# Kernel optimization log

Measured on AMD Instinct MI355X. Metric: run time of the kernel, lower is better.

Reference implementation:

```python
import jax, jax.numpy as jnp
import numpy as np

B, D, CTX, H = 262144, 16, 128, 192
IN_DIM = D + CTX + 1  # 145


def _linear_init(k, fan_in, fan_out):
    bound = 1.0 / np.sqrt(fan_in)
    kw, kb = jax.random.split(k)
    W = jax.random.uniform(kw, (fan_in, fan_out), jnp.float32, -bound, bound)
    b = jax.random.uniform(kb, (fan_out,), jnp.float32, -bound, bound)
    return W, b


def setup_inputs() -> dict:
    key = jax.random.key(0)
    ks = jax.random.split(key, 7)
    W1, b1 = _linear_init(ks[0], IN_DIM, H)
    W2, b2 = _linear_init(ks[1], H, H)
    W3, b3 = _linear_init(ks[2], H, D)
    return {
        "t": jax.random.uniform(ks[3], (), jnp.float32),
        "y": jax.random.normal(ks[4], (B, D), jnp.float32),
        "logp": jnp.zeros((B,), jnp.float32),
        "h": jax.random.normal(ks[5], (B, CTX), jnp.float32),
        "eps": jax.random.normal(ks[6], (B, D), jnp.float32),
        "W1": W1, "b1": b1, "W2": W2, "b2": b2, "W3": W3, "b3": b3,
    }


def _mlp(x, W1, b1, W2, b2, W3, b3):
    # 3-layer MLP, exact (erf) GELU as torch.nn.GELU default
    x = jax.nn.gelu(x @ W1 + b1, approximate=False)
    x = jax.nn.gelu(x @ W2 + b2, approximate=False)
    return x @ W3 + b3


def reference(t, y, logp, h, eps, W1, b1, W2, b2, W3, b3):
    Bsz = y.shape[0]
    t_feat = jnp.ones((Bsz, 1), y.dtype) * t

    def f_of_y(yy):
        inp = jnp.concatenate([yy, h, t_feat], axis=1)  # (B, D+CTX+1)
        return _mlp(inp, W1, b1, W2, b2, W3, b3)  # (B, D)

    # Hutchinson: torch computes g = J^T eps then (g*eps).sum(1) = eps^T J^T eps,
    # which per-row equals eps^T J eps = dot(eps, J eps). Forward-mode JVP computes
    # f and J eps in one fused pass (same math, no explicit backward graph).
    f, Jeps = jax.jvp(f_of_y, (y,), (eps,))
    trace = jnp.sum(Jeps * eps, axis=1)  # (B,)
    dlogp = -trace
    dh = jnp.zeros_like(h)
    return (f, dlogp, dh)
```

## Files before the change

kernel.cpp:

```cpp
#include <hip/hip_runtime.h>
#include <hip/hip_bf16.h>
#include <math.h>

#define B_TOTAL 262144
#define D 16
#define CTX 128
#define H 192
#define KX 192
#define M 32
#define BLOCK 256

typedef __attribute__((ext_vector_type(8))) short bf16x8;
typedef __attribute__((ext_vector_type(4))) float f32x4;

#define MFMA(a, b, c) __builtin_amdgcn_mfma_f32_16x16x32_bf16((a), (b), (c), 0, 0, 0)

__device__ __forceinline__ unsigned short f2bf_rne(float f) {
    unsigned u = __builtin_bit_cast(unsigned, f);
    u += 0x7FFFu + ((u >> 16) & 1u);
    return (unsigned short)(u >> 16);
}
__device__ __forceinline__ void split2(float v, unsigned short& hi, unsigned short& lo) {
    unsigned u = __builtin_bit_cast(unsigned, v);
    hi = (unsigned short)(u >> 16);
    float hf = __builtin_bit_cast(float, u & 0xFFFF0000u);
    lo = f2bf_rne(v - hf);
}
__device__ __forceinline__ void gelu_pair(float x, float& a, float& gp) {
    float e    = __expf(-0.5f * x * x);
    float az   = fabsf(x) * 0.70710678118654752f;
    float t    = __builtin_amdgcn_rcpf(fmaf(0.47047f, az, 1.0f));
    float p    = t * fmaf(t, fmaf(t, 0.7478556f, -0.0958798f), 0.3480242f);
    float erfv = __builtin_copysignf(fmaf(-p, e, 1.0f), x);
    float phi  = fmaf(0.5f, erfv, 0.5f);
    gp = fmaf(0.39894228040143268f * x, e, phi);
    a  = x * phi;
}

__global__ void prep_weights(const float* __restrict__ W1,
                             const float* __restrict__ W2,
                             const float* __restrict__ W3,
                             unsigned short* __restrict__ wt)
{
    int i = blockIdx.x * 256 + threadIdx.x;
    if (i < H * KX) {
        int n = i / KX, kp = i % KX;
        float v = 0.0f;
        if (kp < 16)                       v = W1[kp * H + n];
        else if (kp == 16)                 v = W1[144 * H + n];
        else if (kp >= 32 && kp < 160)     v = W1[(kp - 16) * H + n];
        else if (kp >= 160 && kp < 176)    v = W1[(kp - 160) * H + n];
        else if (kp == 176)                v = W1[144 * H + n];
        wt[i] = f2bf_rne(v);
        return;
    }
    i -= H * KX;
    if (i < H * H) {
        int n = i / H, k = i % H;
        wt[36864 + i] = f2bf_rne(W2[k * H + n]);
        return;
    }
    i -= H * H;
    if (i < D * H) {
        int n = i / H, k = i % H;
        wt[73728 + i] = f2bf_rne(W3[k * D + n]);
    }
}

__global__ __launch_bounds__(BLOCK, 5) void odefunc_mfma(
    const float* __restrict__ t_ptr,
    const float* __restrict__ y,
    const float* __restrict__ h,
    const float* __restrict__ eps,
    const float* __restrict__ b1,
    const float* __restrict__ b2,
    const float* __restrict__ b3,
    const unsigned short* __restrict__ wt,
    float* __restrict__ out_f,
    float* __restrict__ out_dlogp,
    float* __restrict__ out_dh)
{
    __shared__ __align__(16) unsigned char smem[30208];
    unsigned short (*Xh)[200] = (unsigned short (*)[200])smem;
    unsigned short (*Tc)[72]  = (unsigned short (*)[72])(smem + 12800);
    unsigned short (*A)[200]  = (unsigned short (*)[200])smem;
    unsigned short (*U)[200]  = (unsigned short (*)[200])(smem + 17408);

    const int tid  = threadIdx.x;
    const int lane = tid & 63;
    const int wv   = tid >> 6;
    const int quad = lane >> 4;
    const int l16  = lane & 15;
    const size_t r0 = (size_t)blockIdx.x * M;

    const unsigned short* Wt1 = wt;
    const unsigned short* Wt2 = wt + 36864;
    const unsigned short* Wt3 = wt + 73728;

    {
        float4 z4 = {0.f, 0.f, 0.f, 0.f};
        #pragma unroll
        for (int i = 0; i < 4; ++i) {
            int idx = tid + i * BLOCK;
            int r = idx >> 5, c4 = (idx & 31) * 4;
            *(float4*)(out_dh + (r0 + r) * CTX + c4) = z4;
        }
    }

    {
        int task = tid >> 7, idx = tid & 127;
        int r = idx >> 2, d4 = (idx & 3) * 4;
        const float* src = task ? eps : y;
        float4 v = *(const float4*)(src + (r0 + r) * D + d4);
        ushort4 hi, lo;
        split2(v.x, hi.x, lo.x); split2(v.y, hi.y, lo.y);
        split2(v.z, hi.z, lo.z); split2(v.w, hi.w, lo.w);
        if (task == 0) { *(ushort4*)&Xh[r][d4] = hi; *(ushort4*)&Xh[r][160 + d4] = lo; }
        else           { *(ushort4*)&Tc[r][d4] = hi; *(ushort4*)&Tc[r][32 + d4] = lo; }
    }
    if (tid < M) {
        int r = tid;
        float tv = t_ptr[0];
        unsigned short thi, tlo;
        split2(tv, thi, tlo);
        ushort4 z4 = {0, 0, 0, 0};
        ushort4 t4 = {thi, 0, 0, 0};
        ushort4 l4 = {tlo, 0, 0, 0};
        *(ushort4*)&Xh[r][16]  = t4; *(ushort4*)&Xh[r][20]  = z4;
        *(ushort4*)&Xh[r][24]  = z4; *(ushort4*)&Xh[r][28]  = z4;
        *(ushort4*)&Xh[r][176] = l4; *(ushort4*)&Xh[r][180] = z4;
        *(ushort4*)&Xh[r][184] = z4; *(ushort4*)&Xh[r][188] = z4;
        *(ushort4*)&Tc[r][16]  = z4; *(ushort4*)&Tc[r][20]  = z4;
        *(ushort4*)&Tc[r][24]  = z4; *(ushort4*)&Tc[r][28]  = z4;
        *(ushort4*)&Tc[r][48]  = z4; *(ushort4*)&Tc[r][52]  = z4;
        *(ushort4*)&Tc[r][56]  = z4; *(ushort4*)&Tc[r][60]  = z4;
    }
    #pragma unroll
    for (int i = 0; i < 4; ++i) {
        int idx = tid + i * BLOCK;
        int r = idx >> 5, c4 = (idx & 31) * 4;
        float4 v = *(const float4*)(h + (r0 + r) * CTX + c4);
        ushort4 hv = { f2bf_rne(v.x), f2bf_rne(v.y), f2bf_rne(v.z), f2bf_rne(v.w) };
        *(ushort4*)&Xh[r][32 + c4] = hv;
    }
    __syncthreads();

    const f32x4 zf = {0.f, 0.f, 0.f, 0.f};

    f32x4 z[2][3], u[2][3];
    #pragma unroll
    for (int rt = 0; rt < 2; ++rt)
        #pragma unroll
        for (int j = 0; j < 3; ++j) { z[rt][j] = zf; u[rt][j] = zf; }

    bf16x8 w1f[3][6];
    #pragma unroll
    for (int j = 0; j < 3; ++j) {
        int n = (wv * 3 + j) * 16 + l16;
        #pragma unroll
        for (int kc = 0; kc < 6; ++kc)
            w1f[j][kc] = *(const bf16x8*)(Wt1 + n * KX + kc * 32 + quad * 8);
    }
    #pragma unroll
    for (int kc = 0; kc < 6; ++kc)
        #pragma unroll
        for (int rt = 0; rt < 2; ++rt) {
            bf16x8 ah = *(const bf16x8*)&Xh[rt * 16 + l16][kc * 32 + quad * 8];
            #pragma unroll
            for (int j = 0; j < 3; ++j) z[rt][j] = MFMA(ah, w1f[j][kc], z[rt][j]);
        }
    #pragma unroll
    for (int rt = 0; rt < 2; ++rt) {
        int m = rt * 16 + l16;
        bf16x8 th = *(const bf16x8*)&Tc[m][quad * 8];
        bf16x8 tl = *(const bf16x8*)&Tc[m][32 + quad * 8];
        #pragma unroll
        for (int j = 0; j < 3; ++j) {
            u[rt][j] = MFMA(th, w1f[j][0], u[rt][j]);
            u[rt][j] = MFMA(tl, w1f[j][5], u[rt][j]);
        }
    }
    __syncthreads();

    #pragma unroll
    for (int j = 0; j < 3; ++j) {
        int n = (wv * 3 + j) * 16 + l16;
        float bb = b1[n];
        #pragma unroll
        for (int rt = 0; rt < 2; ++rt)
            #pragma unroll
            for (int rg = 0; rg < 4; ++rg) {
                int m = rt * 16 + quad * 4 + rg;
                float x = z[rt][j][rg] + bb;
                float a, gp; gelu_pair(x, a, gp);
                A[m][n] = f2bf_rne(a);
                U[m][n] = f2bf_rne(u[rt][j][rg] * gp);
            }
    }
    __syncthreads();

    f32x4 z2[2][3], u2[2][3];
    #pragma unroll
    for (int rt = 0; rt < 2; ++rt)
        #pragma unroll
        for (int j = 0; j < 3; ++j) { z2[rt][j] = zf; u2[rt][j] = zf; }

    bf16x8 w2f[3][6];
    #pragma unroll
    for (int j = 0; j < 3; ++j) {
        int n = (wv * 3 + j) * 16 + l16;
        #pragma unroll
        for (int kc = 0; kc < 6; ++kc)
            w2f[j][kc] = *(const bf16x8*)(Wt2 + n * H + kc * 32 + quad * 8);
    }
    #pragma unroll
    for (int kc = 0; kc < 6; ++kc)
        #pragma unroll
        for (int rt = 0; rt < 2; ++rt) {
            int m = rt * 16 + l16, o = kc * 32 + quad * 8;
            bf16x8 av = *(const bf16x8*)&A[m][o];
            bf16x8 uv = *(const bf16x8*)&U[m][o];
            #pragma unroll
            for (int j = 0; j < 3; ++j) {
                z2[rt][j] = MFMA(av, w2f[j][kc], z2[rt][j]);
                u2[rt][j] = MFMA(uv, w2f[j][kc], u2[rt][j]);
            }
        }
    __syncthreads();

    #pragma unroll
    for (int j = 0; j < 3; ++j) {
        int n = (wv * 3 + j) * 16 + l16;
        float bb = b2[n];
        #pragma unroll
        for (int rt = 0; rt < 2; ++rt)
            #pragma unroll
            for (int rg = 0; rg < 4; ++rg) {
                int m = rt * 16 + quad * 4 + rg;
                float x = z2[rt][j][rg] + bb;
                float a, gp; gelu_pair(x, a, gp);
                A[m][n] = f2bf_rne(a);
                U[m][n] = f2bf_rne(u2[rt][j][rg] * gp);
            }
    }
    __syncthreads();

    {
        const int strm = wv & 1, rt = wv >> 1;
        const unsigned short (*P)[200] = strm ? U : A;

        bf16x8 w3f[6];
        #pragma unroll
        for (int kc = 0; kc < 6; ++kc)
            w3f[kc] = *(const bf16x8*)(Wt3 + l16 * H + kc * 32 + quad * 8);

        f32x4 acc = zf;
        #pragma unroll
        for (int kc = 0; kc < 6; ++kc) {
            bf16x8 xv = *(const bf16x8*)&P[rt * 16 + l16][kc * 32 + quad * 8];
            acc = MFMA(xv, w3f[kc], acc);
        }

        if (strm == 0) {
            float bb = b3[l16];
            #pragma unroll
            for (int rg = 0; rg < 4; ++rg) {
                int m = rt * 16 + quad * 4 + rg;
                out_f[(r0 + m) * D + l16] = acc[rg] + bb;
            }
        } else {
            float pr[4];
            #pragma unroll
            for (int rg = 0; rg < 4; ++rg) {
                int m = rt * 16 + quad * 4 + rg;
                pr[rg] = acc[rg] * eps[(r0 + m) * D + l16];
            }
            #pragma unroll
            for (int sh = 1; sh < 16; sh <<= 1)
                #pragma unroll
                for (int rg = 0; rg < 4; ++rg)
                    pr[rg] += __shfl_xor(pr[rg], sh, 64);
            if (l16 == 0)
                #pragma unroll
                for (int rg = 0; rg < 4; ++rg)
                    out_dlogp[r0 + rt * 16 + quad * 4 + rg] = -pr[rg];
        }
    }
}

extern "C" void kernel_launch(void* const* d_in, const int* in_sizes, int n_in,
                              void* d_out, int out_size, void* d_ws, size_t ws_size,
                              hipStream_t stream)
{
    const float* t   = (const float*)d_in[0];
    const float* y   = (const float*)d_in[1];
    const float* h   = (const float*)d_in[3];
    const float* eps = (const float*)d_in[4];
    const float* W1  = (const float*)d_in[5];
    const float* b1  = (const float*)d_in[6];
    const float* W2  = (const float*)d_in[7];
    const float* b2  = (const float*)d_in[8];
    const float* W3  = (const float*)d_in[9];
    const float* b3  = (const float*)d_in[10];

    float* out       = (float*)d_out;
    float* out_f     = out;
    float* out_dlogp = out + (size_t)B_TOTAL * D;
    float* out_dh    = out + (size_t)B_TOTAL * (D + 1);

    unsigned short* wt = (unsigned short*)d_ws;

    int prep_elems = H * KX + H * H + D * H;
    prep_weights<<<(prep_elems + 255) / 256, 256, 0, stream>>>(W1, W2, W3, wt);

    odefunc_mfma<<<B_TOTAL / M, BLOCK, 0, stream>>>(
        t, y, h, eps, b1, b2, b3, wt, out_f, out_dlogp, out_dh);
}
```

Before: 417.7 us.

## Fold time feature into bias, add tangent weight block, use persistent grid

Folds the t·W1[144] term into a precomputed layer-1 bias in the prep kernel, so the time column no longer passes through the MFMA input tile. The tangent (eps) stream now shares the input tile and uses a dedicated 32-wide weight block, with A/U buffers separated from the input tile in shared memory. The main kernel becomes a persistent loop over tiles with a fixed grid of 1024 blocks and launch bounds of 4 blocks per CU, and the biases are hoisted into registers. Risks: the weights are still reloaded from global/L2 on every iteration, and the lower occupancy with a single grid wave may reduce latency hiding.

```diff
diff --git a/kernel.cpp b/kernel.cpp
--- a/kernel.cpp
+++ b/kernel.cpp
@@ -9,6 +9,8 @@
 #define KX 192
 #define M 32
 #define BLOCK 256
+#define GRID 1024
+#define NTILE (B_TOTAL / M)
 
 typedef __attribute__((ext_vector_type(8))) short bf16x8;
 typedef __attribute__((ext_vector_type(4))) float f32x4;
@@ -37,7 +39,9 @@
     a  = x * phi;
 }
 
-__global__ void prep_weights(const float* __restrict__ W1,
+__global__ void prep_weights(const float* __restrict__ t_ptr,
+                             const float* __restrict__ W1,
+                             const float* __restrict__ b1,
                              const float* __restrict__ W2,
                              const float* __restrict__ W3,
                              unsigned short* __restrict__ wt)
@@ -46,11 +50,9 @@
     if (i < H * KX) {
         int n = i / KX, kp = i % KX;
         float v = 0.0f;
-        if (kp < 16)                       v = W1[kp * H + n];
-        else if (kp == 16)                 v = W1[144 * H + n];
-        else if (kp >= 32 && kp < 160)     v = W1[(kp - 16) * H + n];
-        else if (kp >= 160 && kp < 176)    v = W1[(kp - 160) * H + n];
-        else if (kp == 176)                v = W1[144 * H + n];
+        if (kp < 16)                    v = W1[kp * H + n];
+        else if (kp >= 32 && kp < 160)  v = W1[(kp - 16) * H + n];
+        else if (kp >= 160 && kp < 176) v = W1[(kp - 160) * H + n];
         wt[i] = f2bf_rne(v);
         return;
     }
@@ -62,17 +64,28 @@
     }
     i -= H * H;
     if (i < D * H) {
-        int n = i / H, k = i % H;
-        wt[73728 + i] = f2bf_rne(W3[k * D + n]);
-    }
-}
-
-__global__ __launch_bounds__(BLOCK, 5) void odefunc_mfma(
-    const float* __restrict__ t_ptr,
+        int d = i / H, k = i % H;
+        wt[73728 + i] = f2bf_rne(W3[k * D + d]);
+        return;
+    }
+    i -= D * H;
+    if (i < H * 32) {
+        int n = i / 32, k = i % 32;
+        float v = (k >= 16) ? W1[(k - 16) * H + n] : 0.0f;
+        wt[76800 + i] = f2bf_rne(v);
+        return;
+    }
+    i -= H * 32;
+    if (i < H) {
+        float* b1p = (float*)(wt + 82944);
+        b1p[i] = b1[i] + t_ptr[0] * W1[144 * H + i];
+    }
+}
+
+__global__ __launch_bounds__(BLOCK, 4) void odefunc_mfma(
     const float* __restrict__ y,
     const float* __restrict__ h,
     const float* __restrict__ eps,
-    const float* __restrict__ b1,
     const float* __restrict__ b2,
     const float* __restrict__ b3,
     const unsigned short* __restrict__ wt,
@@ -80,210 +93,204 @@
     float* __restrict__ out_dlogp,
     float* __restrict__ out_dh)
 {
-    __shared__ __align__(16) unsigned char smem[30208];
-    unsigned short (*Xh)[200] = (unsigned short (*)[200])smem;
-    unsigned short (*Tc)[72]  = (unsigned short (*)[72])(smem + 12800);
-    unsigned short (*A)[200]  = (unsigned short (*)[200])smem;
-    unsigned short (*U)[200]  = (unsigned short (*)[200])(smem + 17408);
+    __shared__ __align__(16) unsigned char smem[38400];
+    unsigned short (*Xc)[200] = (unsigned short (*)[200])smem;
+    unsigned short (*A)[200]  = (unsigned short (*)[200])(smem + 12800);
+    unsigned short (*U)[200]  = (unsigned short (*)[200])(smem + 25600);
 
     const int tid  = threadIdx.x;
     const int lane = tid & 63;
     const int wv   = tid >> 6;
     const int quad = lane >> 4;
     const int l16  = lane & 15;
-    const size_t r0 = (size_t)blockIdx.x * M;
-
-    const unsigned short* Wt1 = wt;
-    const unsigned short* Wt2 = wt + 36864;
-    const unsigned short* Wt3 = wt + 73728;
-
-    {
-        float4 z4 = {0.f, 0.f, 0.f, 0.f};
+
+    const unsigned short* Wt1v = wt;
+    const unsigned short* Wt2  = wt + 36864;
+    const unsigned short* Wt3  = wt + 73728;
+    const unsigned short* Wtan = wt + 76800;
+    const float*          b1p  = (const float*)(wt + 82944);
+
+    float bb1[3], bb2[3];
+    #pragma unroll
+    for (int j = 0; j < 3; ++j) {
+        int n = (wv * 3 + j) * 16 + l16;
+        bb1[j] = b1p[n];
+        bb2[j] = b2[n];
+    }
+    const float bb3 = b3[l16];
+    const f32x4 zf = {0.f, 0.f, 0.f, 0.f};
+
+    for (int it = 0; it < NTILE / GRID; ++it) {
+        const size_t r0 = (size_t)(it * GRID + blockIdx.x) * M;
+
+        {
+            float4 z4 = {0.f, 0.f, 0.f, 0.f};
+            #pragma unroll
+            for (int i = 0; i < 4; ++i) {
+                int idx = tid + i * BLOCK;
+                int r = idx >> 5, c4 = (idx & 31) * 4;
+                *(float4*)(out_dh + (r0 + r) * CTX + c4) = z4;
+            }
+        }
+
+        {
+            int task = tid >> 7, idx = tid & 127;
+            int r = idx >> 2, d4 = (idx & 3) * 4;
+            const float* src = task ? eps : y;
+            float4 v = *(const float4*)(src + (r0 + r) * D + d4);
+            ushort4 hi, lo;
+            split2(v.x, hi.x, lo.x); split2(v.y, hi.y, lo.y);
+            split2(v.z, hi.z, lo.z); split2(v.w, hi.w, lo.w);
+            int c = task * 16 + d4;
+            *(ushort4*)&Xc[r][c] = hi; *(ushort4*)&Xc[r][160 + c] = lo;
+        }
         #pragma unroll
         for (int i = 0; i < 4; ++i) {
             int idx = tid + i * BLOCK;
             int r = idx >> 5, c4 = (idx & 31) * 4;
-            *(float4*)(out_dh + (r0 + r) * CTX + c4) = z4;
-        }
-    }
-
-    {
-        int task = tid >> 7, idx = tid & 127;
-        int r = idx >> 2, d4 = (idx & 3) * 4;
-        const float* src = task ? eps : y;
-        float4 v = *(const float4*)(src + (r0 + r) * D + d4);
-        ushort4 hi, lo;
-        split2(v.x, hi.x, lo.x); split2(v.y, hi.y, lo.y);
-        split2(v.z, hi.z, lo.z); split2(v.w, hi.w, lo.w);
-        if (task == 0) { *(ushort4*)&Xh[r][d4] = hi; *(ushort4*)&Xh[r][160 + d4] = lo; }
-        else           { *(ushort4*)&Tc[r][d4] = hi; *(ushort4*)&Tc[r][32 + d4] = lo; }
-    }
-    if (tid < M) {
-        int r = tid;
-        float tv = t_ptr[0];
-        unsigned short thi, tlo;
-        split2(tv, thi, tlo);
-        ushort4 z4 = {0, 0, 0, 0};
-        ushort4 t4 = {thi, 0, 0, 0};
-        ushort4 l4 = {tlo, 0, 0, 0};
-        *(ushort4*)&Xh[r][16]  = t4; *(ushort4*)&Xh[r][20]  = z4;
-        *(ushort4*)&Xh[r][24]  = z4; *(ushort4*)&Xh[r][28]  = z4;
-        *(ushort4*)&Xh[r][176] = l4; *(ushort4*)&Xh[r][180] = z4;
-        *(ushort4*)&Xh[r][184] = z4; *(ushort4*)&Xh[r][188] = z4;
-        *(ushort4*)&Tc[r][16]  = z4; *(ushort4*)&Tc[r][20]  = z4;
-        *(ushort4*)&Tc[r][24]  = z4; *(ushort4*)&Tc[r][28]  = z4;
-        *(ushort4*)&Tc[r][48]  = z4; *(ushort4*)&Tc[r][52]  = z4;
-        *(ushort4*)&Tc[r][56]  = z4; *(ushort4*)&Tc[r][60]  = z4;
-    }
-    #pragma unroll
-    for (int i = 0; i < 4; ++i) {
-        int idx = tid + i * BLOCK;
-        int r = idx >> 5, c4 = (idx & 31) * 4;
-        float4 v = *(const float4*)(h + (r0 + r) * CTX + c4);
-        ushort4 hv = { f2bf_rne(v.x), f2bf_rne(v.y), f2bf_rne(v.z), f2bf_rne(v.w) };
-        *(ushort4*)&Xh[r][32 + c4] = hv;
-    }
-    __syncthreads();
-
-    const f32x4 zf = {0.f, 0.f, 0.f, 0.f};
-
-    f32x4 z[2][3], u[2][3];
-    #pragma unroll
-    for (int rt = 0; rt < 2; ++rt)
-        #pragma unroll
-        for (int j = 0; j < 3; ++j) { z[rt][j] = zf; u[rt][j] = zf; }
-
-    bf16x8 w1f[3][6];
-    #pragma unroll
-    for (int j = 0; j < 3; ++j) {
-        int n = (wv * 3 + j) * 16 + l16;
+            float4 v = *(const float4*)(h + (r0 + r) * CTX + c4);
+            ushort4 hv = { f2bf_rne(v.x), f2bf_rne(v.y), f2bf_rne(v.z), f2bf_rne(v.w) };
+            *(ushort4*)&Xc[r][32 + c4] = hv;
+        }
+        __syncthreads();
+
+        f32x4 z[2][3], u[2][3];
+        #pragma unroll
+        for (int rt = 0; rt < 2; ++rt)
+            #pragma unroll
+            for (int j = 0; j < 3; ++j) { z[rt][j] = zf; u[rt][j] = zf; }
+
+        bf16x8 w1f[3][6], wtf[3];
+        #pragma unroll
+        for (int j = 0; j < 3; ++j) {
+            int n = (wv * 3 + j) * 16 + l16;
+            #pragma unroll
+            for (int kc = 0; kc < 6; ++kc)
+                w1f[j][kc] = *(const bf16x8*)(Wt1v + n * KX + kc * 32 + quad * 8);
+            wtf[j] = *(const bf16x8*)(Wtan + n * 32 + quad * 8);
+        }
+        #pragma unroll
+        for (int rt = 0; rt < 2; ++rt) {
+            int m = rt * 16 + l16;
+            bf16x8 a0 = *(const bf16x8*)&Xc[m][quad * 8];
+            #pragma unroll
+            for (int j = 0; j < 3; ++j) {
+                z[rt][j] = MFMA(a0, w1f[j][0], z[rt][j]);
+                u[rt][j] = MFMA(a0, wtf[j],    u[rt][j]);
+            }
+            #pragma unroll
+            for (int kc = 1; kc < 5; ++kc) {
+                bf16x8 ah = *(const bf16x8*)&Xc[m][kc * 32 + quad * 8];
+                #pragma unroll
+                for (int j = 0; j < 3; ++j) z[rt][j] = MFMA(ah, w1f[j][kc], z[rt][j]);
+            }
+            bf16x8 a5 = *(const bf16x8*)&Xc[m][5 * 32 + quad * 8];
+            #pragma unroll
+            for (int j = 0; j < 3; ++j) {
+                z[rt][j] = MFMA(a5, w1f[j][5], z[rt][j]);
+                u[rt][j] = MFMA(a5, wtf[j],    u[rt][j]);
+            }
+        }
+        #pragma unroll
+        for (int j = 0; j < 3; ++j) {
+            int n = (wv * 3 + j) * 16 + l16;
+            #pragma unroll
+            for (int rt = 0; rt < 2; ++rt)
+                #pragma unroll
+                for (int rg = 0; rg < 4; ++rg) {
+                    int m = rt * 16 + quad * 4 + rg;
+                    float x = z[rt][j][rg] + bb1[j];
+                    float a, gp; gelu_pair(x, a, gp);
+                    A[m][n] = f2bf_rne(a);
+                    U[m][n] = f2bf_rne(u[rt][j][rg] * gp);
+                }
+        }
+        __syncthreads();
+
+        f32x4 z2[2][3], u2[2][3];
+        #pragma unroll
+        for (int rt = 0; rt < 2; ++rt)
+            #pragma unroll
+            for (int j = 0; j < 3; ++j) { z2[rt][j] = zf; u2[rt][j] = zf; }
+
+        bf16x8 w2f[3][6];
+        #pragma unroll
+        for (int j = 0; j < 3; ++j) {
+            int n = (wv * 3 + j) * 16 + l16;
+            #pragma unroll
+            for (int kc = 0; kc < 6; ++kc)
+                w2f[j][kc] = *(const bf16x8*)(Wt2 + n * H + kc * 32 + quad * 8);
+        }
         #pragma unroll
         for (int kc = 0; kc < 6; ++kc)
-            w1f[j][kc] = *(const bf16x8*)(Wt1 + n * KX + kc * 32 + quad * 8);
-    }
-    #pragma unroll
-    for (int kc = 0; kc < 6; ++kc)
-        #pragma unroll
-        for (int rt = 0; rt < 2; ++rt) {
-            bf16x8 ah = *(const bf16x8*)&Xh[rt * 16 + l16][kc * 32 + quad * 8];
-            #pragma unroll
-            for (int j = 0; j < 3; ++j) z[rt][j] = MFMA(ah, w1f[j][kc], z[rt][j]);
-        }
-    #pragma unroll
-    for (int rt = 0; rt < 2; ++rt) {
-        int m = rt * 16 + l16;
-        bf16x8 th = *(const bf16x8*)&Tc[m][quad * 8];
-        bf16x8 tl = *(const bf16x8*)&Tc[m][32 + quad * 8];
+            #pragma unroll
+            for (int rt = 0; rt < 2; ++rt) {
+                int m = rt * 16 + l16, o = kc * 32 + quad * 8;
+                bf16x8 av = *(const bf16x8*)&A[m][o];
+                bf16x8 uv = *(const bf16x8*)&U[m][o];
+                #pragma unroll
+                for (int j = 0; j < 3; ++j) {
+                    z2[rt][j] = MFMA(av, w2f[j][kc], z2[rt][j]);
+                    u2[rt][j] = MFMA(uv, w2f[j][kc], u2[rt][j]);
+                }
+            }
+        __syncthreads();
+
         #pragma unroll
         for (int j = 0; j < 3; ++j) {
-            u[rt][j] = MFMA(th, w1f[j][0], u[rt][j]);
-            u[rt][j] = MFMA(tl, w1f[j][5], u[rt][j]);
-        }
-    }
-    __syncthreads();
-
-    #pragma unroll
-    for (int j = 0; j < 3; ++j) {
-        int n = (wv * 3 + j) * 16 + l16;
-        float bb = b1[n];
-        #pragma unroll
-        for (int rt = 0; rt < 2; ++rt)
-            #pragma unroll
-            for (int rg = 0; rg < 4; ++rg) {
-                int m = rt * 16 + quad * 4 + rg;
-                float x = z[rt][j][rg] + bb;
-                float a, gp; gelu_pair(x, a, gp);
-                A[m][n] = f2bf_rne(a);
-                U[m][n] = f2bf_rne(u[rt][j][rg] * gp);
-            }
-    }
-    __syncthreads();
-
-    f32x4 z2[2][3], u2[2][3];
-    #pragma unroll
-    for (int rt = 0; rt < 2; ++rt)
-        #pragma unroll
-        for (int j = 0; j < 3; ++j) { z2[rt][j] = zf; u2[rt][j] = zf; }
-
-    bf16x8 w2f[3][6];
-    #pragma unroll
-    for (int j = 0; j < 3; ++j) {
-        int n = (wv * 3 + j) * 16 + l16;
-        #pragma unroll
-        for (int kc = 0; kc < 6; ++kc)
-            w2f[j][kc] = *(const bf16x8*)(Wt2 + n * H + kc * 32 + quad * 8);
-    }
-    #pragma unroll
-    for (int kc = 0; kc < 6; ++kc)
-        #pragma unroll
-        for (int rt = 0; rt < 2; ++rt) {
-            int m = rt * 16 + l16, o = kc * 32 + quad * 8;
-            bf16x8 av = *(const bf16x8*)&A[m][o];
-            bf16x8 uv = *(const bf16x8*)&U[m][o];
-            #pragma unroll
-            for (int j = 0; j < 3; ++j) {
-                z2[rt][j] = MFMA(av, w2f[j][kc], z2[rt][j]);
-                u2[rt][j] = MFMA(uv, w2f[j][kc], u2[rt][j]);
-            }
-        }
-    __syncthreads();
-
-    #pragma unroll
-    for (int j = 0; j < 3; ++j) {
-        int n = (wv * 3 + j) * 16 + l16;
-        float bb = b2[n];
-        #pragma unroll
-        for (int rt = 0; rt < 2; ++rt)
-            #pragma unroll
-            for (int rg = 0; rg < 4; ++rg) {
-                int m = rt * 16 + quad * 4 + rg;
-                float x = z2[rt][j][rg] + bb;
-                float a, gp; gelu_pair(x, a, gp);
-                A[m][n] = f2bf_rne(a);
-                U[m][n] = f2bf_rne(u2[rt][j][rg] * gp);
-            }
-    }
-    __syncthreads();
-
-    {
-        const int strm = wv & 1, rt = wv >> 1;
-        const unsigned short (*P)[200] = strm ? U : A;
-
-        bf16x8 w3f[6];
-        #pragma unroll
-        for (int kc = 0; kc < 6; ++kc)
-            w3f[kc] = *(const bf16x8*)(Wt3 + l16 * H + kc * 32 + quad * 8);
-
-        f32x4 acc = zf;
-        #pragma unroll
-        for (int kc = 0; kc < 6; ++kc) {
-            bf16x8 xv = *(const bf16x8*)&P[rt * 16 + l16][kc * 32 + quad * 8];
-            acc = MFMA(xv, w3f[kc], acc);
-        }
-
-        if (strm == 0) {
-            float bb = b3[l16];
-            #pragma unroll
-            for (int rg = 0; rg < 4; ++rg) {
-                int m = rt * 16 + quad * 4 + rg;
-                out_f[(r0 + m) * D + l16] = acc[rg] + bb;
-            }
-        } else {
-            float pr[4];
-            #pragma unroll
-            for (int rg = 0; rg < 4; ++rg) {
-                int m = rt * 16 + quad * 4 + rg;
-                pr[rg] = acc[rg] * eps[(r0 + m) * D + l16];
-            }
-            #pragma unroll
-            for (int sh = 1; sh < 16; sh <<= 1)
-                #pragma unroll
-                for (int rg = 0; rg < 4; ++rg)
-                    pr[rg] += __shfl_xor(pr[rg], sh, 64);
-            if (l16 == 0)
-                #pragma unroll
-                for (int rg = 0; rg < 4; ++rg)
-                    out_dlogp[r0 + rt * 16 + quad * 4 + rg] = -pr[rg];
+            int n = (wv * 3 + j) * 16 + l16;
+            #pragma unroll
+            for (int rt = 0; rt < 2; ++rt)
+                #pragma unroll
+                for (int rg = 0; rg < 4; ++rg) {
+                    int m = rt * 16 + quad * 4 + rg;
+                    float x = z2[rt][j][rg] + bb2[j];
+                    float a, gp; gelu_pair(x, a, gp);
+                    A[m][n] = f2bf_rne(a);
+                    U[m][n] = f2bf_rne(u2[rt][j][rg] * gp);
+                }
+        }
+        __syncthreads();
+
+        {
+            const int strm = wv & 1, rt = wv >> 1;
+            const unsigned short (*P)[200] = strm ? U : A;
+
+            bf16x8 w3f[6];
+            #pragma unroll
+            for (int kc = 0; kc < 6; ++kc)
+                w3f[kc] = *(const bf16x8*)(Wt3 + l16 * H + kc * 32 + quad * 8);
+
+            f32x4 acc = zf;
+            #pragma unroll
+            for (int kc = 0; kc < 6; ++kc) {
+                bf16x8 xv = *(const bf16x8*)&P[rt * 16 + l16][kc * 32 + quad * 8];
+                acc = MFMA(xv, w3f[kc], acc);
+            }
+
+            if (strm == 0) {
+                #pragma unroll
+                for (int rg = 0; rg < 4; ++rg) {
+                    int m = rt * 16 + quad * 4 + rg;
+                    out_f[(r0 + m) * D + l16] = acc[rg] + bb3;
+                }
+            } else {
+                float pr[4];
+                #pragma unroll
+                for (int rg = 0; rg < 4; ++rg) {
+                    int m = rt * 16 + quad * 4 + rg;
+                    pr[rg] = acc[rg] * eps[(r0 + m) * D + l16];
+                }
+                #pragma unroll
+                for (int sh = 1; sh < 16; sh <<= 1)
+                    #pragma unroll
+                    for (int rg = 0; rg < 4; ++rg)
+                        pr[rg] += __shfl_xor(pr[rg], sh, 64);
+                if (l16 == 0)
+                    #pragma unroll
+                    for (int rg = 0; rg < 4; ++rg)
+                        out_dlogp[r0 + rt * 16 + quad * 4 + rg] = -pr[rg];
+            }
         }
     }
 }
@@ -310,9 +317,9 @@
 
     unsigned short* wt = (unsigned short*)d_ws;
 
-    int prep_elems = H * KX + H * H + D * H;
-    prep_weights<<<(prep_elems + 255) / 256, 256, 0, stream>>>(W1, W2, W3, wt);
-
-    odefunc_mfma<<<B_TOTAL / M, BLOCK, 0, stream>>>(
-        t, y, h, eps, b1, b2, b3, wt, out_f, out_dlogp, out_dh);
-}
+    int prep_elems = H * KX + H * H + D * H + H * 32 + H;
+    prep_weights<<<(prep_elems + 255) / 256, 256, 0, stream>>>(t, W1, b1, W2, W3, wt);
+
+    odefunc_mfma<<<GRID, BLOCK, 0, stream>>>(
+        y, h, eps, b2, b3, wt, out_f, out_dlogp, out_dh);
+}
```

New measurement: 702.3 us. 68.1% more time.
